# Kernel tuning notes

Measured on AMD Instinct MI355X. Metric: run time of the kernel, lower is better.

The kernel has to match this reference:

```python
import jax, jax.numpy as jnp
import numpy as np

PATCH = 8

def _conv2d(x, w, b, groups=1, pad=0):
    out = jax.lax.conv_general_dilated(
        x, w, window_strides=(1, 1), padding=[(pad, pad), (pad, pad)],
        dimension_numbers=('NCHW', 'OIHW', 'NCHW'), feature_group_count=groups)
    return out + b[None, :, None, None]

def setup_inputs() -> dict:
    key = jax.random.key(0)
    ks = jax.random.split(key, 9)
    B, C, H, W = 8, 32, 256, 256
    C2 = 2 * C
    x = jax.random.normal(ks[0], (B, C, H, W), jnp.float32)
    w_in = jax.random.normal(ks[1], (C2, C, 1, 1), jnp.float32) * 0.1
    b_in = jax.random.normal(ks[2], (C2,), jnp.float32) * 0.01
    fft1 = 1.0 + 0.1 * jax.random.normal(ks[3], (C2, 1, 1, PATCH, PATCH // 2 + 1), jnp.float32)
    fft2 = 1.0 + 0.1 * jax.random.normal(ks[4], (C2, 1, 1, PATCH, PATCH // 2 + 1), jnp.float32)
    w_dw = jax.random.normal(ks[5], (C2, 1, 7, 7), jnp.float32) * 0.05
    b_dw = jax.random.normal(ks[6], (C2,), jnp.float32) * 0.01
    w_out = jax.random.normal(ks[7], (C, C2, 1, 1), jnp.float32) * 0.1
    b_out = jax.random.normal(ks[8], (C,), jnp.float32) * 0.01
    return {'x': x, 'w_in': w_in, 'b_in': b_in, 'fft1': fft1, 'fft2': fft2,
            'w_dw': w_dw, 'b_dw': b_dw, 'w_out': w_out, 'b_out': b_out}

def reference(x, w_in, b_in, fft1, fft2, w_dw, b_dw, w_out, b_out):
    B, C, H, W = x.shape
    C2 = 2 * C
    # 1x1 conv in: C -> 2C
    x = _conv2d(x, w_in, b_in)
    # rearrange b c (h p1) (w p2) -> b c h w p1 p2
    Hp, Wp = H // PATCH, W // PATCH
    xp = x.reshape(B, C2, Hp, PATCH, Wp, PATCH).transpose(0, 1, 2, 4, 3, 5)
    # per-patch 2D rFFT (norm='backward' = default) and learnable spectral filter
    f = jnp.fft.rfft2(xp.astype(jnp.float32)) * fft1  # [B,C2,Hp,Wp,8,5] complex
    y = jax.nn.gelu(jnp.concatenate([f.real, f.imag], axis=1), approximate=False)
    yr, yi = jnp.split(y, 2, axis=1)
    f2 = jax.lax.complex(yr, yi) * fft2
    xp = jnp.fft.irfft2(f2, s=(PATCH, PATCH))  # [B,C2,Hp,Wp,8,8]
    x = xp.transpose(0, 1, 2, 4, 3, 5).reshape(B, C2, H, W)
    # 7x7 depthwise conv + GELU + 1x1 conv out: 2C -> C
    x = _conv2d(x, w_dw, b_dw, groups=C2, pad=3)
    x = jax.nn.gelu(x, approximate=False)
    x = _conv2d(x, w_out, b_out)
    return x
```

## Files before the change

kernel.cpp:

```cpp
#include <hip/hip_runtime.h>
#include <math.h>

#define C_IN 32
#define C2C 64
#define HH 256
#define WW 256

#define R2 0.70710678118654752f

__device__ __forceinline__ float gelu_f(float x) {
    float u = x * R2;
    float a = fabsf(u);
    float t = __builtin_amdgcn_rcpf(fmaf(0.3275911f, a, 1.0f));
    float p = t * fmaf(t, fmaf(t, fmaf(t, fmaf(t, 1.061405429f, -1.453152027f),
                                       1.421413741f), -0.284496736f), 0.254829592f);
    float e = __expf(-a * a);
    float er = fmaf(-p, e, 1.0f);
    er = copysignf(er, u);
    return 0.5f * x * (1.0f + er);
}

__device__ const float CT8d[8] = {1.0f, R2, 0.0f, -R2, -1.0f, -R2, 0.0f, R2};
__device__ const float ST8d[8] = {0.0f, R2, 1.0f, R2, 0.0f, -R2, -1.0f, -R2};

__device__ __forceinline__ void rdft8(const float t[8], float Ar[5], float Ai[5]) {
    float e0 = t[0] + t[4], e1 = t[1] + t[5], e2 = t[2] + t[6], e3 = t[3] + t[7];
    float s04 = t[0] - t[4], s26 = t[2] - t[6];
    float am = t[1] - t[3] - t[5] + t[7];
    float bm = t[1] + t[3] - t[5] - t[7];
    float e02 = e0 + e2, e13 = e1 + e3;
    Ar[0] = e02 + e13;
    Ar[4] = e02 - e13;
    Ar[2] = e0 - e2;
    Ai[2] = e3 - e1;
    float ma = R2 * am, mb = R2 * bm;
    Ar[1] = s04 + ma;
    Ar[3] = s04 - ma;
    Ai[1] = -s26 - mb;
    Ai[3] = s26 - mb;
    Ai[0] = 0.f;
    Ai[4] = 0.f;
}

__device__ __forceinline__ void wrA5(float* ubuf, int c2x, int l,
                                     const float Ar[5], const float Ai[5]) {
    float* pr = &ubuf[c2x * 44 + l];
    float* pi = &ubuf[2816 + c2x * 44 + l];
    pr[0]  = Ar[0];  pi[0]  = 0.f;
    pr[8]  = Ar[1];  pi[8]  = Ai[1];
    pr[16] = Ar[2];  pi[16] = Ai[2];
    pr[24] = Ar[3];  pi[24] = Ai[3];
    pr[32] = Ar[4];  pi[32] = 0.f;
}

__device__ __forceinline__ void colpass(const float* ubuf, int c2x, int l,
                                        const float* __restrict__ fft1,
                                        const float* __restrict__ fft2,
                                        float gr[5], float gi[5]) {
    constexpr float CT[8] = {1.0f, R2, 0.0f, -R2, -1.0f, -R2, 0.0f, R2};
    constexpr float ST[8] = {0.0f, R2, 1.0f, R2, 0.0f, -R2, -1.0f, -R2};
    const int row = (l <= 4) ? l : 8 - l;
    const float sgn = (l <= 4) ? 1.0f : -1.0f;
    float Ar2[8], Ai2[8];
    {
        const float4 r0 = *(const float4*)&ubuf[c2x * 44 + row * 8];
        const float4 r1 = *(const float4*)&ubuf[c2x * 44 + row * 8 + 4];
        const float4 i0 = *(const float4*)&ubuf[2816 + c2x * 44 + row * 8];
        const float4 i1 = *(const float4*)&ubuf[2816 + c2x * 44 + row * 8 + 4];
        Ar2[0] = r0.x; Ar2[1] = r0.y; Ar2[2] = r0.z; Ar2[3] = r0.w;
        Ar2[4] = r1.x; Ar2[5] = r1.y; Ar2[6] = r1.z; Ar2[7] = r1.w;
        Ai2[0] = sgn * i0.x; Ai2[1] = sgn * i0.y; Ai2[2] = sgn * i0.z; Ai2[3] = sgn * i0.w;
        Ai2[4] = sgn * i1.x; Ai2[5] = sgn * i1.y; Ai2[6] = sgn * i1.z; Ai2[7] = sgn * i1.w;
    }
    #pragma unroll
    for (int v = 0; v < 5; ++v) {
        float fr = 0.f, fi = 0.f;
        #pragma unroll
        for (int w = 0; w < 8; ++w) {
            const int k = (v * w) & 7;
            fr += Ar2[w] * CT[k] + Ai2[w] * ST[k];
            fi += Ai2[w] * CT[k] - Ar2[w] * ST[k];
        }
        const float s1 = fft1[(c2x * 8 + l) * 5 + v];
        const float s2 = fft2[(c2x * 8 + l) * 5 + v];
        gr[v] = gelu_f(fr * s1) * s2;
        gi[v] = gelu_f(fi * s1) * s2;
    }
}

__device__ __forceinline__ void invpass(const float* gtab, float c1, float s1, float o[8]) {
    constexpr float CT[8] = {1.0f, R2, 0.0f, -R2, -1.0f, -R2, 0.0f, R2};
    constexpr float ST[8] = {0.0f, R2, 1.0f, R2, 0.0f, -R2, -1.0f, -R2};
    float Rr[5] = {0.f, 0.f, 0.f, 0.f, 0.f};
    float Ri[5] = {0.f, 0.f, 0.f, 0.f, 0.f};
    float cu = 1.f, su = 0.f;
    #pragma unroll
    for (int u = 0; u < 8; ++u) {
        const float4 g0 = *(const float4*)&gtab[u * 12];
        const float4 g1 = *(const float4*)&gtab[u * 12 + 4];
        const float2 g2 = *(const float2*)&gtab[u * 12 + 8];
        Rr[0] += g0.x * cu - g0.y * su;  Ri[0] += g0.x * su + g0.y * cu;
        Rr[1] += g0.z * cu - g0.w * su;  Ri[1] += g0.z * su + g0.w * cu;
        Rr[2] += g1.x * cu - g1.y * su;  Ri[2] += g1.x * su + g1.y * cu;
        Rr[3] += g1.z * cu - g1.w * su;  Ri[3] += g1.z * su + g1.w * cu;
        Rr[4] += g2.x * cu - g2.y * su;  Ri[4] += g2.x * su + g2.y * cu;
        const float nc = cu * c1 - su * s1;
        su = cu * s1 + su * c1;
        cu = nc;
    }
    #pragma unroll
    for (int w = 0; w < 8; ++w) {
        float s = 0.f;
        #pragma unroll
        for (int v = 0; v < 5; ++v) {
            const float m = (v == 0 || v == 4) ? 1.0f : 2.0f;
            const int k = (v * w) & 7;
            s += m * (Rr[v] * CT[k] - Ri[v] * ST[k]);
        }
        o[w] = s * 0.015625f;
    }
}

__global__ __launch_bounds__(256, 4)
void k1_spectral(const float* __restrict__ x, const float* __restrict__ w_in,
                 const float* __restrict__ b_in, const float* __restrict__ fft1,
                 const float* __restrict__ fft2, float* __restrict__ z)
{
    __shared__ __align__(16) float ubuf[6400];

    const int tid = threadIdx.x;
    const int c2 = tid >> 3;
    const int l  = tid & 7;

    int Lf = blockIdx.x + (blockIdx.y << 5) + (blockIdx.z << 10);
    int Lp = ((Lf & 7) << 10) | (Lf >> 3);
    const int b  = Lp >> 10;
    const int hp = (Lp >> 5) & 31;
    const int wp = Lp & 31;
    const int h0 = hp << 3, w0 = wp << 3;

    #pragma unroll
    for (int k = 0; k < 2; ++k) {
        int i = tid + (k << 8);
        int c = i >> 4, rem = i & 15;
        int h = rem >> 1, half = rem & 1;
        const float4 v = *(const float4*)&x[((b * C_IN + c) * HH + h0 + h) * WW + w0 + (half << 2)];
        int base = c * 100 + half * 48 + h;
        ubuf[base]      = v.x;
        ubuf[base + 12] = v.y;
        ubuf[base + 24] = v.z;
        ubuf[base + 36] = v.w;
    }
    #pragma unroll
    for (int k = 0; k < 2; ++k) {
        int i = tid + (k << 8);
        int ci = i >> 3, c4 = (i & 7) << 2;
        const float4 v = *(const float4*)&w_in[ci * C_IN + c4];
        int col = ((ci & 31) << 1) | (ci >> 5);
        ubuf[3200 + (c4 + 0) * 66 + col] = v.x;
        ubuf[3200 + (c4 + 1) * 66 + col] = v.y;
        ubuf[3200 + (c4 + 2) * 66 + col] = v.z;
        ubuf[3200 + (c4 + 3) * 66 + col] = v.w;
    }
    __syncthreads();

    float t0[8], t1[8];
    {
        const float bv0 = b_in[c2], bv1 = b_in[c2 + 32];
        #pragma unroll
        for (int h = 0; h < 8; ++h) { t0[h] = bv0; t1[h] = bv1; }
        #pragma unroll
        for (int c = 0; c < C_IN; ++c) {
            const float2 wv = *(const float2*)&ubuf[3200 + c * 66 + (c2 << 1)];
            const float4 xa = *(const float4*)&ubuf[c * 100 + l * 12];
            const float4 xb = *(const float4*)&ubuf[c * 100 + l * 12 + 4];
            float xv[8];
            xv[0] = xa.x; xv[1] = xa.y; xv[2] = xa.z; xv[3] = xa.w;
            xv[4] = xb.x; xv[5] = xb.y; xv[6] = xb.z; xv[7] = xb.w;
            #pragma unroll
            for (int h = 0; h < 8; ++h) {
                t0[h] = fmaf(wv.x, xv[h], t0[h]);
                t1[h] = fmaf(wv.y, xv[h], t1[h]);
            }
        }
    }

    float Ar_a[5], Ai_a[5], Ar_b[5], Ai_b[5];
    rdft8(t0, Ar_a, Ai_a);
    rdft8(t1, Ar_b, Ai_b);
    __syncthreads();
    wrA5(ubuf, c2,      l, Ar_a, Ai_a);
    wrA5(ubuf, c2 + 32, l, Ar_b, Ai_b);
    __syncthreads();

    float gr_a[5], gi_a[5], gr_b[5], gi_b[5];
    colpass(ubuf, c2,      l, fft1, fft2, gr_a, gi_a);
    colpass(ubuf, c2 + 32, l, fft1, fft2, gr_b, gi_b);
    __syncthreads();
    {
        int gb = c2 * 100 + l * 12;
        *(float4*)&ubuf[gb]     = make_float4(gr_a[0], gi_a[0], gr_a[1], gi_a[1]);
        *(float4*)&ubuf[gb + 4] = make_float4(gr_a[2], gi_a[2], gr_a[3], gi_a[3]);
        *(float2*)&ubuf[gb + 8] = make_float2(gr_a[4], gi_a[4]);
        gb = (c2 + 32) * 100 + l * 12;
        *(float4*)&ubuf[gb]     = make_float4(gr_b[0], gi_b[0], gr_b[1], gi_b[1]);
        *(float4*)&ubuf[gb + 4] = make_float4(gr_b[2], gi_b[2], gr_b[3], gi_b[3]);
        *(float2*)&ubuf[gb + 8] = make_float2(gr_b[4], gi_b[4]);
    }
    __syncthreads();

    const float c1 = CT8d[l], s1 = ST8d[l];
    float o[8];
    const int pbase = (((b * C2C) * 1024) + hp * 32 + wp) << 6;
    invpass(&ubuf[c2 * 100], c1, s1, o);
    {
        float* zp = &z[pbase + (c2 << 16) + (l << 3)];
        *(float4*)&zp[0] = make_float4(o[0], o[1], o[2], o[3]);
        *(float4*)&zp[4] = make_float4(o[4], o[5], o[6], o[7]);
    }
    invpass(&ubuf[(c2 + 32) * 100], c1, s1, o);
    {
        float* zp = &z[pbase + ((c2 + 32) << 16) + (l << 3)];
        *(float4*)&zp[0] = make_float4(o[0], o[1], o[2], o[3]);
        *(float4*)&zp[4] = make_float4(o[4], o[5], o[6], o[7]);
    }
}

__global__ __launch_bounds__(256, 4)
void k2_dwconv(const float* __restrict__ z, const float* __restrict__ w_dw,
               const float* __restrict__ b_dw, const float* __restrict__ w_out,
               const float* __restrict__ b_out, float* __restrict__ out)
{
    __shared__ __align__(16) float zs[4 * 22 * 32];
    __shared__ __align__(16) float gbuf[4 * 16 * 32];

    const int tid = threadIdx.x;

    int L = blockIdx.x + (blockIdx.y << 4) + (blockIdx.z << 8);
    int Lp = ((L & 7) << 8) | (L >> 3);
    const int b  = Lp >> 8;
    const int ty = (Lp >> 4) & 15;
    const int tx = Lp & 15;
    const int x0g = tx << 4, y0g = ty << 4;

    const int lane = tid & 63;
    const int wv   = tid >> 6;
    const int bx   = lane >> 4;
    const int oy   = lane & 15;

    const int ox = tid & 15, py = tid >> 4;

    const float *zsrc0, *zsrc1, *zsrc2;
    int zdst0, zdst1, zdst2;
    bool zin0, zin1, zin2;
    bool zact2;
    {
        #define MK_SLOT(K, SRC, DST, INB, ACT)                                  \
        {                                                                        \
            const int i   = tid + (K << 8);                                      \
            const bool ac = (i < 528);                                           \
            const int c2l = i / 132;                                             \
            const int r   = i - c2l * 132;                                       \
            const int yy  = r / 6;                                               \
            const int x4  = r - yy * 6;                                          \
            const int gy  = y0g - 3 + yy;                                        \
            const int gx  = x0g - 4 + (x4 << 2);                                 \
            INB = ac && ((unsigned)gy < HH) && ((unsigned)gx < WW);              \
            const int hp  = (gy >> 3) & 31;                                      \
            const int wpp = (gx >> 3) & 31;                                      \
            const int off = ((gy & 7) << 3) | (gx & 7);                          \
            SRC = z + ((((b * C2C + (c2l & 3)) * 1024 + hp * 32 + wpp) << 6) + off); \
            DST = (c2l & 3) * 704 + (yy % 22) * 32 + ((x4 ^ (yy & 7)) << 2);     \
            ACT = ac;                                                            \
        }
        bool dummy0, dummy1;
        MK_SLOT(0, zsrc0, zdst0, zin0, dummy0)
        MK_SLOT(1, zsrc1, zdst1, zin1, dummy1)
        MK_SLOT(2, zsrc2, zdst2, zin2, zact2)
        (void)dummy0; (void)dummy1;
        #undef MK_SLOT
    }

    const float4 zero4 = make_float4(0.f, 0.f, 0.f, 0.f);

    float4 pf0 = zin0 ? *(const float4*)(zsrc0) : zero4;
    float4 pf1 = zin1 ? *(const float4*)(zsrc1) : zero4;
    float4 pf2 = zin2 ? *(const float4*)(zsrc2) : zero4;

    float acc[32];
    #pragma unroll
    for (int c = 0; c < 32; ++c) acc[c] = b_out[c];

    for (int chunk = 0; chunk < 16; ++chunk) {
        const int cbase = chunk << 2;
        __syncthreads();

        *(float4*)&zs[zdst0] = pf0;
        *(float4*)&zs[zdst1] = pf1;
        if (zact2) *(float4*)&zs[zdst2] = pf2;

        if (chunk < 15) {
            const int coff = (chunk + 1) << 18;
            pf0 = zin0 ? *(const float4*)(zsrc0 + coff) : zero4;
            pf1 = zin1 ? *(const float4*)(zsrc1 + coff) : zero4;
            pf2 = zin2 ? *(const float4*)(zsrc2 + coff) : zero4;
        }
        __syncthreads();

        {
            const int c2u = __builtin_amdgcn_readfirstlane(cbase + wv);
            const float* wd = &w_dw[c2u * 49];
            const float bd = b_dw[c2u];
            float a0 = bd, a1 = bd, a2 = bd, a3 = bd;
            const float* zch = &zs[wv * 704];
            #pragma unroll
            for (int ky = 0; ky < 7; ++ky) {
                const int row = oy + ky;
                const int rs = row & 7;
                const float* zr = &zch[row * 32];
                const float4 q0 = *(const float4*)&zr[((bx ^ rs) << 2)];
                const float4 q1 = *(const float4*)&zr[(((bx + 1) ^ rs) << 2)];
                const float4 q2 = *(const float4*)&zr[(((bx + 2) ^ rs) << 2)];
                const float fv[11] = {q0.x, q0.y, q0.z, q0.w, q1.x, q1.y, q1.z, q1.w,
                                      q2.x, q2.y, q2.z};
                #pragma unroll
                for (int kx = 0; kx < 7; ++kx) {
                    const float w = wd[ky * 7 + kx];
                    a0 = fmaf(w, fv[kx + 1], a0);
                    a1 = fmaf(w, fv[kx + 2], a1);
                    a2 = fmaf(w, fv[kx + 3], a2);
                    a3 = fmaf(w, fv[kx + 4], a3);
                }
            }
            *(float4*)&gbuf[wv * 512 + oy * 32 + ((bx ^ (oy & 7)) << 2)] =
                make_float4(gelu_f(a0), gelu_f(a1), gelu_f(a2), gelu_f(a3));
        }
        __syncthreads();

        {
            const int sw = (((ox >> 2) ^ (py & 7)) << 2) | (ox & 3);
            #pragma unroll
            for (int cc = 0; cc < 4; ++cc) {
                const float gv = gbuf[cc * 512 + py * 32 + sw];
                const int c2i = cbase + cc;
                #pragma unroll
                for (int c = 0; c < 32; ++c)
                    acc[c] = fmaf(w_out[c * C2C + c2i], gv, acc[c]);
            }
        }
    }

    #pragma unroll
    for (int c = 0; c < 32; ++c)
        out[((b * C_IN + c) * HH + y0g + py) * WW + x0g + ox] = acc[c];
}

extern "C" void kernel_launch(void* const* d_in, const int* in_sizes, int n_in,
                              void* d_out, int out_size, void* d_ws, size_t ws_size,
                              hipStream_t stream) {
    const float* x     = (const float*)d_in[0];
    const float* w_in  = (const float*)d_in[1];
    const float* b_in  = (const float*)d_in[2];
    const float* fft1  = (const float*)d_in[3];
    const float* fft2  = (const float*)d_in[4];
    const float* w_dw  = (const float*)d_in[5];
    const float* b_dw  = (const float*)d_in[6];
    const float* w_out = (const float*)d_in[7];
    const float* b_out = (const float*)d_in[8];
    float* outp = (float*)d_out;
    float* z = (float*)d_ws;

    dim3 g1(32, 32, 8);
    k1_spectral<<<g1, 256, 0, stream>>>(x, w_in, b_in, fft1, fft2, z);
    dim3 g2(16, 16, 8);
    k2_dwconv<<<g2, 256, 0, stream>>>(z, w_dw, b_dw, w_out, b_out, outp);
}
```

Measured before the change: 343.5 us.

## Double the dwconv tile height so each thread computes two output rows

The depthwise-conv plus 1x1-out kernel now processes 16x32 output tiles instead of 16x16. Each thread computes two adjacent rows, reusing each loaded shared-memory row for both, and the pointwise stage reuses each w_out load across two pixels. This cuts halo reloads and weight loads per output. The prefetch of the next channel chunk moves after the depthwise compute to overlap with the later stage, and the gbuf swizzle changes. The cost is higher register pressure from 64 accumulators plus the prefetch registers under launch_bounds(256,4), more shared memory per block, and half as many blocks.

```diff
diff --git a/kernel.cpp b/kernel.cpp
--- a/kernel.cpp
+++ b/kernel.cpp
@@ -231,36 +231,36 @@
                const float* __restrict__ b_dw, const float* __restrict__ w_out,
                const float* __restrict__ b_out, float* __restrict__ out)
 {
-    __shared__ __align__(16) float zs[4 * 22 * 32];
-    __shared__ __align__(16) float gbuf[4 * 16 * 32];
+    __shared__ __align__(16) float zs[4 * 38 * 32];
+    __shared__ __align__(16) float gbuf[4 * 32 * 32];
 
     const int tid = threadIdx.x;
 
-    int L = blockIdx.x + (blockIdx.y << 4) + (blockIdx.z << 8);
-    int Lp = ((L & 7) << 8) | (L >> 3);
-    const int b  = Lp >> 8;
-    const int ty = (Lp >> 4) & 15;
+    int L = blockIdx.x + (blockIdx.y << 4) + (blockIdx.z << 7);
+    int Lp = ((L & 7) << 7) | (L >> 3);
+    const int b  = Lp >> 7;
+    const int ty = (Lp >> 4) & 7;
     const int tx = Lp & 15;
-    const int x0g = tx << 4, y0g = ty << 4;
+    const int x0g = tx << 4, y0g = ty << 5;
 
     const int lane = tid & 63;
     const int wv   = tid >> 6;
     const int bx   = lane >> 4;
-    const int oy   = lane & 15;
+    const int oyp  = lane & 15;
 
     const int ox = tid & 15, py = tid >> 4;
 
-    const float *zsrc0, *zsrc1, *zsrc2;
-    int zdst0, zdst1, zdst2;
-    bool zin0, zin1, zin2;
-    bool zact2;
-    {
-        #define MK_SLOT(K, SRC, DST, INB, ACT)                                  \
+    const float *zsrc0, *zsrc1, *zsrc2, *zsrc3;
+    int zdst0, zdst1, zdst2, zdst3;
+    bool zin0, zin1, zin2, zin3;
+    const bool zact3 = (tid < 144);
+    {
+        #define MK_SLOT(K, SRC, DST, INB)                                        \
         {                                                                        \
             const int i   = tid + (K << 8);                                      \
-            const bool ac = (i < 528);                                           \
-            const int c2l = i / 132;                                             \
-            const int r   = i - c2l * 132;                                       \
+            const bool ac = (i < 912);                                           \
+            const int c2l = i / 228;                                             \
+            const int r   = i - c2l * 228;                                       \
             const int yy  = r / 6;                                               \
             const int x4  = r - yy * 6;                                          \
             const int gy  = y0g - 3 + yy;                                        \
@@ -270,14 +270,12 @@
             const int wpp = (gx >> 3) & 31;                                      \
             const int off = ((gy & 7) << 3) | (gx & 7);                          \
             SRC = z + ((((b * C2C + (c2l & 3)) * 1024 + hp * 32 + wpp) << 6) + off); \
-            DST = (c2l & 3) * 704 + (yy % 22) * 32 + ((x4 ^ (yy & 7)) << 2);     \
-            ACT = ac;                                                            \
-        }
-        bool dummy0, dummy1;
-        MK_SLOT(0, zsrc0, zdst0, zin0, dummy0)
-        MK_SLOT(1, zsrc1, zdst1, zin1, dummy1)
-        MK_SLOT(2, zsrc2, zdst2, zin2, zact2)
-        (void)dummy0; (void)dummy1;
+            DST = (c2l & 3) * 1216 + yy * 32 + ((x4 ^ (yy & 7)) << 2);           \
+        }
+        MK_SLOT(0, zsrc0, zdst0, zin0)
+        MK_SLOT(1, zsrc1, zdst1, zin1)
+        MK_SLOT(2, zsrc2, zdst2, zin2)
+        MK_SLOT(3, zsrc3, zdst3, zin3)
         #undef MK_SLOT
     }
 
@@ -286,10 +284,11 @@
     float4 pf0 = zin0 ? *(const float4*)(zsrc0) : zero4;
     float4 pf1 = zin1 ? *(const float4*)(zsrc1) : zero4;
     float4 pf2 = zin2 ? *(const float4*)(zsrc2) : zero4;
-
-    float acc[32];
-    #pragma unroll
-    for (int c = 0; c < 32; ++c) acc[c] = b_out[c];
+    float4 pf3 = zin3 ? *(const float4*)(zsrc3) : zero4;
+
+    float acc0[32], acc1[32];
+    #pragma unroll
+    for (int c = 0; c < 32; ++c) { const float bv = b_out[c]; acc0[c] = bv; acc1[c] = bv; }
 
     for (int chunk = 0; chunk < 16; ++chunk) {
         const int cbase = chunk << 2;
@@ -297,25 +296,20 @@
 
         *(float4*)&zs[zdst0] = pf0;
         *(float4*)&zs[zdst1] = pf1;
-        if (zact2) *(float4*)&zs[zdst2] = pf2;
-
-        if (chunk < 15) {
-            const int coff = (chunk + 1) << 18;
-            pf0 = zin0 ? *(const float4*)(zsrc0 + coff) : zero4;
-            pf1 = zin1 ? *(const float4*)(zsrc1 + coff) : zero4;
-            pf2 = zin2 ? *(const float4*)(zsrc2 + coff) : zero4;
-        }
+        *(float4*)&zs[zdst2] = pf2;
+        if (zact3) *(float4*)&zs[zdst3] = pf3;
         __syncthreads();
 
         {
             const int c2u = __builtin_amdgcn_readfirstlane(cbase + wv);
             const float* wd = &w_dw[c2u * 49];
             const float bd = b_dw[c2u];
-            float a0 = bd, a1 = bd, a2 = bd, a3 = bd;
-            const float* zch = &zs[wv * 704];
+            float s0 = bd, s1 = bd, s2 = bd, s3 = bd;
+            float u0 = bd, u1 = bd, u2 = bd, u3 = bd;
+            const float* zch = &zs[wv * 1216];
             #pragma unroll
-            for (int ky = 0; ky < 7; ++ky) {
-                const int row = oy + ky;
+            for (int rr = 0; rr < 8; ++rr) {
+                const int row = (oyp << 1) + rr;
                 const int rs = row & 7;
                 const float* zr = &zch[row * 32];
                 const float4 q0 = *(const float4*)&zr[((bx ^ rs) << 2)];
@@ -323,36 +317,67 @@
                 const float4 q2 = *(const float4*)&zr[(((bx + 2) ^ rs) << 2)];
                 const float fv[11] = {q0.x, q0.y, q0.z, q0.w, q1.x, q1.y, q1.z, q1.w,
                                       q2.x, q2.y, q2.z};
-                #pragma unroll
-                for (int kx = 0; kx < 7; ++kx) {
-                    const float w = wd[ky * 7 + kx];
-                    a0 = fmaf(w, fv[kx + 1], a0);
-                    a1 = fmaf(w, fv[kx + 2], a1);
-                    a2 = fmaf(w, fv[kx + 3], a2);
-                    a3 = fmaf(w, fv[kx + 4], a3);
+                if (rr < 7) {
+                    const float* wr = &wd[rr * 7];
+                    #pragma unroll
+                    for (int kx = 0; kx < 7; ++kx) {
+                        const float w = wr[kx];
+                        s0 = fmaf(w, fv[kx + 1], s0);
+                        s1 = fmaf(w, fv[kx + 2], s1);
+                        s2 = fmaf(w, fv[kx + 3], s2);
+                        s3 = fmaf(w, fv[kx + 4], s3);
+                    }
+                }
+                if (rr > 0) {
+                    const float* wr = &wd[(rr - 1) * 7];
+                    #pragma unroll
+                    for (int kx = 0; kx < 7; ++kx) {
+                        const float w = wr[kx];
+                        u0 = fmaf(w, fv[kx + 1], u0);
+                        u1 = fmaf(w, fv[kx + 2], u1);
+                        u2 = fmaf(w, fv[kx + 3], u2);
+                        u3 = fmaf(w, fv[kx + 4], u3);
+                    }
                 }
             }
-            *(float4*)&gbuf[wv * 512 + oy * 32 + ((bx ^ (oy & 7)) << 2)] =
-                make_float4(gelu_f(a0), gelu_f(a1), gelu_f(a2), gelu_f(a3));
+            const int r0 = oyp << 1, r1 = r0 + 1;
+            *(float4*)&gbuf[wv * 1024 + r0 * 32 + ((bx ^ ((r0 & 3) << 1)) << 2)] =
+                make_float4(gelu_f(s0), gelu_f(s1), gelu_f(s2), gelu_f(s3));
+            *(float4*)&gbuf[wv * 1024 + r1 * 32 + ((bx ^ ((r1 & 3) << 1)) << 2)] =
+                make_float4(gelu_f(u0), gelu_f(u1), gelu_f(u2), gelu_f(u3));
+        }
+
+        if (chunk < 15) {
+            const int coff = (chunk + 1) << 18;
+            pf0 = zin0 ? *(const float4*)(zsrc0 + coff) : zero4;
+            pf1 = zin1 ? *(const float4*)(zsrc1 + coff) : zero4;
+            pf2 = zin2 ? *(const float4*)(zsrc2 + coff) : zero4;
+            pf3 = zin3 ? *(const float4*)(zsrc3 + coff) : zero4;
         }
         __syncthreads();
 
         {
-            const int sw = (((ox >> 2) ^ (py & 7)) << 2) | (ox & 3);
+            const int gw = (((ox >> 2) ^ ((py & 3) << 1)) << 2) | (ox & 3);
             #pragma unroll
             for (int cc = 0; cc < 4; ++cc) {
-                const float gv = gbuf[cc * 512 + py * 32 + sw];
+                const float gv0 = gbuf[cc * 1024 + py * 32 + gw];
+                const float gv1 = gbuf[cc * 1024 + (py + 16) * 32 + gw];
                 const int c2i = cbase + cc;
                 #pragma unroll
-                for (int c = 0; c < 32; ++c)
-                    acc[c] = fmaf(w_out[c * C2C + c2i], gv, acc[c]);
+                for (int c = 0; c < 32; ++c) {
+                    const float wv_ = w_out[c * C2C + c2i];
+                    acc0[c] = fmaf(wv_, gv0, acc0[c]);
+                    acc1[c] = fmaf(wv_, gv1, acc1[c]);
+                }
             }
         }
     }
 
     #pragma unroll
-    for (int c = 0; c < 32; ++c)
-        out[((b * C_IN + c) * HH + y0g + py) * WW + x0g + ox] = acc[c];
+    for (int c = 0; c < 32; ++c) {
+        out[((b * C_IN + c) * HH + y0g + py) * WW + x0g + ox]      = acc0[c];
+        out[((b * C_IN + c) * HH + y0g + py + 16) * WW + x0g + ox] = acc1[c];
+    }
 }
 
 extern "C" void kernel_launch(void* const* d_in, const int* in_sizes, int n_in,
@@ -372,6 +397,6 @@
 
     dim3 g1(32, 32, 8);
     k1_spectral<<<g1, 256, 0, stream>>>(x, w_in, b_in, fft1, fft2, z);
-    dim3 g2(16, 16, 8);
+    dim3 g2(16, 8, 8);
     k2_dwconv<<<g2, 256, 0, stream>>>(z, w_dw, b_dw, w_out, b_out, outp);
 }
```

Result: slower. 595.5 us (+73.3%).
